# Kernel optimization log

Measured on AMD Instinct MI355X. Metric: run time of the kernel, lower is better.

Reference implementation:

```python
import jax, jax.numpy as jnp
import numpy as np

E, D_MODEL, D_HIDDEN, TOK_PER_EXP = 64, 1024, 4096, 128


def setup_inputs() -> dict:
    key = jax.random.key(0)
    k1, k2, k3 = jax.random.split(key, 3)
    n_tokens = E * TOK_PER_EXP  # 8192
    inputs = jax.random.normal(k1, (n_tokens, D_MODEL), dtype=jnp.float32)
    # torch nn.Linear weights are [out_features, in_features]
    w1 = jax.random.normal(k2, (E, D_HIDDEN, D_MODEL), dtype=jnp.float32) * (1.0 / np.sqrt(D_MODEL))
    w2 = jax.random.normal(k3, (E, D_MODEL, D_HIDDEN), dtype=jnp.float32) * (1.0 / np.sqrt(D_HIDDEN))
    splits = np.full((E,), TOK_PER_EXP, dtype=np.int64)  # concrete host-side sizes, as in torch .tolist()
    return {"inputs": inputs, "w1": w1, "w2": w2, "splits": splits}


def reference(inputs, w1, w2, splits):
    # splits is a concrete (host) int array: chunk sizes along token dim, expert i uses splits[i % E].
    sizes = [int(s) for s in np.asarray(splits)]
    offsets = np.concatenate([[0], np.cumsum(sizes)])
    n_exp = w1.shape[0]
    outs = []
    for i, m in enumerate(sizes):  # loop over fixed expert list (structurally distinct weights)
        e = i % n_exp
        x = jax.lax.dynamic_slice_in_dim(inputs, int(offsets[i]), m, axis=0)  # [m, d_model]
        h = jax.nn.relu(x @ w1[e].T)          # [m, d_hidden]
        outs.append(h @ w2[e].T)              # [m, d_model]
    return jnp.concatenate(outs, axis=0)       # [N, d_model]
```

## Files before the change

kernel.cpp:

```cpp
#include <hip/hip_runtime.h>
#include <hip/hip_bf16.h>


typedef __attribute__((ext_vector_type(8))) short bf16x8;
typedef __attribute__((ext_vector_type(4))) float f32x4;

#define N_EXPERTS 64
#define DM 1024
#define DH 4096
#define TOKS 128

__device__ __forceinline__ unsigned short f2bf(float f) {
    union { float f; unsigned u; } v; v.f = f;
    unsigned r = v.u + 0x7FFFu + ((v.u >> 16) & 1u);
    return (unsigned short)(r >> 16);
}

template<int N, int K, bool A_BF16, bool RELU_OUT_BF16>
__global__ __launch_bounds__(256, 2)
void moe_gemm(const void* __restrict__ Ap, const float* __restrict__ Bp,
              void* __restrict__ Cp, int nwg_per_xcd)
{
    constexpr int BK = 32;
    constexpr int NT = K / BK;
    constexpr int NTILES = N / 128;

    __shared__ unsigned short sA[2][128][BK];
    __shared__ unsigned short sB[2][128][BK];

    const int tid = threadIdx.x;
    const int bid = (blockIdx.x & 7) * nwg_per_xcd + (blockIdx.x >> 3);
    const int e   = bid / NTILES;
    const int nt  = bid % NTILES;

    const int lane = tid & 63;
    const int w    = tid >> 6;
    const int wr   = w >> 1;
    const int wc   = w & 1;
    const int lrow = lane & 15;
    const int kq   = lane >> 4;

    const float* Bbase = Bp + (size_t)e * N * K + (size_t)nt * 128 * K;

    const float*          Af = nullptr;
    const unsigned short* Ah = nullptr;
    if constexpr (A_BF16) Ah = (const unsigned short*)Ap + (size_t)e * TOKS * K;
    else                  Af = (const float*)Ap + (size_t)e * TOKS * K;

    const int srow = tid >> 3;
    const int sc4  = tid & 7;
    const int hrow = tid >> 2;
    const int hc8  = tid & 3;

    struct Regs {
        float4 b[4];
        float4 af[4];
        uint4  ah[2];
    };
    Regs r0, r1;

    f32x4 acc[4][4];
    #pragma unroll
    for (int i = 0; i < 4; ++i)
        #pragma unroll
        for (int n = 0; n < 4; ++n)
            #pragma unroll
            for (int q = 0; q < 4; ++q) acc[i][n][q] = 0.f;

    auto LOAD = [&](int t, Regs& r) {
        const int k0 = t * BK;
        #pragma unroll
        for (int j = 0; j < 4; ++j)
            r.b[j] = *(const float4*)(Bbase + (size_t)(srow + j * 32) * K + k0 + sc4 * 4);
        if constexpr (A_BF16) {
            #pragma unroll
            for (int j = 0; j < 2; ++j)
                r.ah[j] = *(const uint4*)(Ah + (size_t)(hrow + j * 64) * K + k0 + hc8 * 8);
        } else {
            #pragma unroll
            for (int j = 0; j < 4; ++j)
                r.af[j] = *(const float4*)(Af + (size_t)(srow + j * 32) * K + k0 + sc4 * 4);
        }
    };

    auto WRITE = [&](int buf, Regs& r) {
        #pragma unroll
        for (int j = 0; j < 4; ++j) {
            ushort4 p;
            p.x = f2bf(r.b[j].x); p.y = f2bf(r.b[j].y);
            p.z = f2bf(r.b[j].z); p.w = f2bf(r.b[j].w);
            *(ushort4*)&sB[buf][srow + j * 32][sc4 * 4] = p;
        }
        if constexpr (A_BF16) {
            #pragma unroll
            for (int j = 0; j < 2; ++j)
                *(uint4*)&sA[buf][hrow + j * 64][hc8 * 8] = r.ah[j];
        } else {
            #pragma unroll
            for (int j = 0; j < 4; ++j) {
                ushort4 p;
                p.x = f2bf(r.af[j].x); p.y = f2bf(r.af[j].y);
                p.z = f2bf(r.af[j].z); p.w = f2bf(r.af[j].w);
                *(ushort4*)&sA[buf][srow + j * 32][sc4 * 4] = p;
            }
        }
    };

    auto COMPUTE = [&](int buf) {
        bf16x8 af[4], bfr[4];
        #pragma unroll
        for (int i = 0; i < 4; ++i)
            af[i] = *(const bf16x8*)&sA[buf][wr * 64 + i * 16 + lrow][kq * 8];
        #pragma unroll
        for (int n = 0; n < 4; ++n)
            bfr[n] = *(const bf16x8*)&sB[buf][wc * 64 + n * 16 + lrow][kq * 8];
        #pragma unroll
        for (int i = 0; i < 4; ++i)
            #pragma unroll
            for (int n = 0; n < 4; ++n)
                acc[i][n] = __builtin_amdgcn_mfma_f32_16x16x32_bf16(af[i], bfr[n], acc[i][n], 0, 0, 0);
    };

    LOAD(0, r0);
    LOAD(1, r1);
    WRITE(0, r0);
    asm volatile("s_waitcnt lgkmcnt(0)" ::: "memory");
    __builtin_amdgcn_s_barrier();

    for (int t = 0; t < NT; t += 2) {
        if (t + 2 < NT) LOAD(t + 2, r0);
        COMPUTE(0);
        if (t + 1 < NT) WRITE(1, r1);
        asm volatile("s_waitcnt lgkmcnt(0)" ::: "memory");
        __builtin_amdgcn_s_barrier();

        if (t + 3 < NT) LOAD(t + 3, r1);
        COMPUTE(1);
        if (t + 2 < NT) WRITE(0, r0);
        asm volatile("s_waitcnt lgkmcnt(0)" ::: "memory");
        __builtin_amdgcn_s_barrier();
    }

    const size_t crow0 = (size_t)e * TOKS;
    if constexpr (RELU_OUT_BF16) {
        unsigned short* C = (unsigned short*)Cp;
        #pragma unroll
        for (int i = 0; i < 4; ++i)
            #pragma unroll
            for (int n = 0; n < 4; ++n)
                #pragma unroll
                for (int q = 0; q < 4; ++q) {
                    const int row = wr * 64 + i * 16 + kq * 4 + q;
                    const int col = nt * 128 + wc * 64 + n * 16 + lrow;
                    C[(crow0 + row) * N + col] = f2bf(fmaxf(acc[i][n][q], 0.f));
                }
    } else {
        float* C = (float*)Cp;
        #pragma unroll
        for (int i = 0; i < 4; ++i)
            #pragma unroll
            for (int n = 0; n < 4; ++n)
                #pragma unroll
                for (int q = 0; q < 4; ++q) {
                    const int row = wr * 64 + i * 16 + kq * 4 + q;
                    const int col = nt * 128 + wc * 64 + n * 16 + lrow;
                    C[(crow0 + row) * N + col] = acc[i][n][q];
                }
    }
}

extern "C" void kernel_launch(void* const* d_in, const int* in_sizes, int n_in,
                              void* d_out, int out_size, void* d_ws, size_t ws_size,
                              hipStream_t stream) {
    const float* inputs = (const float*)d_in[0];
    const float* w1     = (const float*)d_in[1];
    const float* w2     = (const float*)d_in[2];

    unsigned short* h = (unsigned short*)d_ws;
    float* out = (float*)d_out;

    moe_gemm<DH, DM, false, true><<<dim3(N_EXPERTS * (DH / 128)), dim3(256), 0, stream>>>(
        inputs, w1, h, N_EXPERTS * (DH / 128) / 8);
    moe_gemm<DM, DH, true, false><<<dim3(N_EXPERTS * (DM / 128)), dim3(256), 0, stream>>>(
        h, w2, out, N_EXPERTS * (DM / 128) / 8);
}
```

Baseline: 539.6 us.

## Pre-convert activations to bf16, double BK, and swizzle LDS tiles

Adds a separate kernel that converts the fp32 input activations to bf16 once, so the first GEMM reads bf16 activations instead of converting them in every N-tile workgroup. The GEMM K-tile grows from 32 to 64. Each thread now loads one contiguous half-row per tile, and shared-memory chunks are XOR-swizzled to avoid LDS bank conflicts when MFMA fragments are read. The trade-offs are an extra launch and a round trip of the converted input through workspace memory, plus more live registers per thread, which could hurt occupancy.

Result: slower. 707.2 us (+31.1%).

```diff
diff --git a/kernel.cpp b/kernel.cpp
--- a/kernel.cpp
+++ b/kernel.cpp
@@ -16,12 +16,25 @@
     return (unsigned short)(r >> 16);
 }
 
-template<int N, int K, bool A_BF16, bool RELU_OUT_BF16>
+__global__ __launch_bounds__(256)
+void cvt_bf16(const float* __restrict__ in, unsigned short* __restrict__ outp, int n8) {
+    int i = blockIdx.x * blockDim.x + threadIdx.x;
+    if (i >= n8) return;
+    const float4* p = (const float4*)in + (size_t)i * 2;
+    float4 a = p[0], b = p[1];
+    ushort4 lo, hi;
+    lo.x = f2bf(a.x); lo.y = f2bf(a.y); lo.z = f2bf(a.z); lo.w = f2bf(a.w);
+    hi.x = f2bf(b.x); hi.y = f2bf(b.y); hi.z = f2bf(b.z); hi.w = f2bf(b.w);
+    ushort4* q = (ushort4*)outp + (size_t)i * 2;
+    q[0] = lo; q[1] = hi;
+}
+
+template<int N, int K, bool RELU_OUT_BF16>
 __global__ __launch_bounds__(256, 2)
-void moe_gemm(const void* __restrict__ Ap, const float* __restrict__ Bp,
+void moe_gemm(const unsigned short* __restrict__ Ab, const float* __restrict__ Bp,
               void* __restrict__ Cp, int nwg_per_xcd)
 {
-    constexpr int BK = 32;
+    constexpr int BK = 64;
     constexpr int NT = K / BK;
     constexpr int NTILES = N / 128;
 
@@ -40,24 +53,16 @@
     const int lrow = lane & 15;
     const int kq   = lane >> 4;
 
-    const float* Bbase = Bp + (size_t)e * N * K + (size_t)nt * 128 * K;
+    const int srow = tid >> 1;
+    const int shalf = tid & 1;
+    const int sswz = (srow >> 1) & 7;
 
-    const float*          Af = nullptr;
-    const unsigned short* Ah = nullptr;
-    if constexpr (A_BF16) Ah = (const unsigned short*)Ap + (size_t)e * TOKS * K;
-    else                  Af = (const float*)Ap + (size_t)e * TOKS * K;
+    const unsigned short* aRow = Ab + (size_t)(e * TOKS + srow) * K;
+    const float*          bRow = Bp + ((size_t)e * N + (size_t)nt * 128 + srow) * K;
 
-    const int srow = tid >> 3;
-    const int sc4  = tid & 7;
-    const int hrow = tid >> 2;
-    const int hc8  = tid & 3;
-
-    struct Regs {
-        float4 b[4];
-        float4 af[4];
-        uint4  ah[2];
-    };
-    Regs r0, r1;
+    const int sl = (lrow >> 1) & 7;
+    const int offk0 = ((0 * 4 + kq) ^ sl) * 8;
+    const int offk1 = ((1 * 4 + kq) ^ sl) * 8;
 
     f32x4 acc[4][4];
     #pragma unroll
@@ -67,58 +72,59 @@
             #pragma unroll
             for (int q = 0; q < 4; ++q) acc[i][n][q] = 0.f;
 
+    struct Regs {
+        uint4  a[4];
+        float4 b[8];
+    };
+    Regs r0, r1;
+
     auto LOAD = [&](int t, Regs& r) {
-        const int k0 = t * BK;
+        const unsigned short* ap = aRow + t * BK + shalf * 32;
         #pragma unroll
-        for (int j = 0; j < 4; ++j)
-            r.b[j] = *(const float4*)(Bbase + (size_t)(srow + j * 32) * K + k0 + sc4 * 4);
-        if constexpr (A_BF16) {
-            #pragma unroll
-            for (int j = 0; j < 2; ++j)
-                r.ah[j] = *(const uint4*)(Ah + (size_t)(hrow + j * 64) * K + k0 + hc8 * 8);
-        } else {
-            #pragma unroll
-            for (int j = 0; j < 4; ++j)
-                r.af[j] = *(const float4*)(Af + (size_t)(srow + j * 32) * K + k0 + sc4 * 4);
-        }
+        for (int i = 0; i < 4; ++i)
+            r.a[i] = *(const uint4*)(ap + i * 8);
+        const float* bp = bRow + t * BK + shalf * 32;
+        #pragma unroll
+        for (int i = 0; i < 8; ++i)
+            r.b[i] = *(const float4*)(bp + i * 4);
     };
 
     auto WRITE = [&](int buf, Regs& r) {
         #pragma unroll
-        for (int j = 0; j < 4; ++j) {
-            ushort4 p;
-            p.x = f2bf(r.b[j].x); p.y = f2bf(r.b[j].y);
-            p.z = f2bf(r.b[j].z); p.w = f2bf(r.b[j].w);
-            *(ushort4*)&sB[buf][srow + j * 32][sc4 * 4] = p;
+        for (int i = 0; i < 4; ++i) {
+            const int c = (shalf * 4 + i) ^ sswz;
+            *(uint4*)&sA[buf][srow][c * 8] = r.a[i];
         }
-        if constexpr (A_BF16) {
-            #pragma unroll
-            for (int j = 0; j < 2; ++j)
-                *(uint4*)&sA[buf][hrow + j * 64][hc8 * 8] = r.ah[j];
-        } else {
-            #pragma unroll
-            for (int j = 0; j < 4; ++j) {
-                ushort4 p;
-                p.x = f2bf(r.af[j].x); p.y = f2bf(r.af[j].y);
-                p.z = f2bf(r.af[j].z); p.w = f2bf(r.af[j].w);
-                *(ushort4*)&sA[buf][srow + j * 32][sc4 * 4] = p;
-            }
+        #pragma unroll
+        for (int i = 0; i < 4; ++i) {
+            const int c = (shalf * 4 + i) ^ sswz;
+            uint4 u;
+            float4 lo = r.b[i * 2], hi = r.b[i * 2 + 1];
+            u.x = (unsigned)f2bf(lo.x) | ((unsigned)f2bf(lo.y) << 16);
+            u.y = (unsigned)f2bf(lo.z) | ((unsigned)f2bf(lo.w) << 16);
+            u.z = (unsigned)f2bf(hi.x) | ((unsigned)f2bf(hi.y) << 16);
+            u.w = (unsigned)f2bf(hi.z) | ((unsigned)f2bf(hi.w) << 16);
+            *(uint4*)&sB[buf][srow][c * 8] = u;
         }
     };
 
     auto COMPUTE = [&](int buf) {
-        bf16x8 af[4], bfr[4];
         #pragma unroll
-        for (int i = 0; i < 4; ++i)
-            af[i] = *(const bf16x8*)&sA[buf][wr * 64 + i * 16 + lrow][kq * 8];
-        #pragma unroll
-        for (int n = 0; n < 4; ++n)
-            bfr[n] = *(const bf16x8*)&sB[buf][wc * 64 + n * 16 + lrow][kq * 8];
-        #pragma unroll
-        for (int i = 0; i < 4; ++i)
+        for (int kh = 0; kh < 2; ++kh) {
+            const int off = kh ? offk1 : offk0;
+            bf16x8 af[4], bfr[4];
+            #pragma unroll
+            for (int i = 0; i < 4; ++i)
+                af[i] = *(const bf16x8*)&sA[buf][wr * 64 + i * 16 + lrow][off];
             #pragma unroll
             for (int n = 0; n < 4; ++n)
-                acc[i][n] = __builtin_amdgcn_mfma_f32_16x16x32_bf16(af[i], bfr[n], acc[i][n], 0, 0, 0);
+                bfr[n] = *(const bf16x8*)&sB[buf][wc * 64 + n * 16 + lrow][off];
+            #pragma unroll
+            for (int i = 0; i < 4; ++i)
+                #pragma unroll
+                for (int n = 0; n < 4; ++n)
+                    acc[i][n] = __builtin_amdgcn_mfma_f32_16x16x32_bf16(af[i], bfr[n], acc[i][n], 0, 0, 0);
+        }
     };
 
     LOAD(0, r0);
@@ -176,11 +182,15 @@
     const float* w1     = (const float*)d_in[1];
     const float* w2     = (const float*)d_in[2];
 
-    unsigned short* h = (unsigned short*)d_ws;
+    unsigned short* h  = (unsigned short*)d_ws;
+    unsigned short* xb = (unsigned short*)((char*)d_ws + (size_t)64 * 1024 * 1024);
     float* out = (float*)d_out;
 
-    moe_gemm<DH, DM, false, true><<<dim3(N_EXPERTS * (DH / 128)), dim3(256), 0, stream>>>(
-        inputs, w1, h, N_EXPERTS * (DH / 128) / 8);
-    moe_gemm<DM, DH, true, false><<<dim3(N_EXPERTS * (DM / 128)), dim3(256), 0, stream>>>(
+    const int n8 = (TOKS * N_EXPERTS) * DM / 8;
+    cvt_bf16<<<dim3(n8 / 256), dim3(256), 0, stream>>>(inputs, xb, n8);
+
+    moe_gemm<DH, DM, true><<<dim3(N_EXPERTS * (DH / 128)), dim3(256), 0, stream>>>(
+        xb, w1, h, N_EXPERTS * (DH / 128) / 8);
+    moe_gemm<DM, DH, false><<<dim3(N_EXPERTS * (DM / 128)), dim3(256), 0, stream>>>(
         h, w2, out, N_EXPERTS * (DM / 128) / 8);
 }
```
